# Kernel tuning notes

Hardware: AMD Instinct MI355X
Metric: run time of the kernel (lower is better)

The kernel has to match this reference:

```python
import jax, jax.numpy as jnp
import numpy as np

B, S, T = 128, 512, 256


def setup_inputs() -> dict:
    key = jax.random.key(0)
    k1, k2, k3, k4 = jax.random.split(key, 4)
    emissions = jax.random.normal(k1, (B, S, T), dtype=jnp.float32)
    mask = jnp.ones((B, S), dtype=bool)
    transitions = jax.random.normal(k2, (T, T), dtype=jnp.float32)
    start_transitions = jax.random.normal(k3, (T,), dtype=jnp.float32)
    end_transitions = jax.random.normal(k4, (T,), dtype=jnp.float32)
    return {
        "emissions": emissions,
        "mask": mask,
        "transitions": transitions,
        "start_transitions": start_transitions,
        "end_transitions": end_transitions,
    }


def reference(emissions, mask, transitions, start_transitions, end_transitions):
    """Batched Viterbi decode. Returns (paths [B,S] int32, best_scores [B] f32).

    Faithful to CRFLayer._viterbi_decode: score_0 = start + em_0; at each step
    next[i,j] = score[i] + trans[i,j] + em_t[j], take max/argmax over i; add
    end_transitions at the end; backtrack via backpointers. Masked (padded)
    steps carry score through unchanged with identity backpointers, so padded
    tail positions replicate the last valid tag (mask is all-ones here, so
    output equals the original's full-length paths).
    """
    Bn, Sn, Tn = emissions.shape
    ident = jnp.arange(Tn, dtype=jnp.int32)
    score0 = start_transitions[None, :] + emissions[:, 0]  # [B,T]

    em_ts = jnp.swapaxes(emissions, 0, 1)[1:]  # [S-1,B,T]
    m_ts = jnp.swapaxes(mask, 0, 1)[1:]        # [S-1,B]

    def step(score, inp):
        em_t, m_t = inp
        # nxt[b,i,j] = score[b,i] + trans[i,j] + em_t[b,j]
        nxt = score[:, :, None] + transitions[None, :, :] + em_t[:, None, :]
        best = jnp.max(nxt, axis=1)                    # [B,T]
        idx = jnp.argmax(nxt, axis=1).astype(jnp.int32)  # [B,T] best prev tag
        m = m_t[:, None]
        new_score = jnp.where(m, best, score)
        bp = jnp.where(m, idx, ident[None, :])
        return new_score, bp

    final_score, history = jax.lax.scan(step, score0, (em_ts, m_ts))  # history [S-1,B,T]
    final_score = final_score + end_transitions[None, :]
    best_scores = jnp.max(final_score, axis=1)                         # [B]
    last_tag = jnp.argmax(final_score, axis=1).astype(jnp.int32)       # [B]

    def back(tag, hist_t):
        prev = jnp.take_along_axis(hist_t, tag[:, None], axis=1)[:, 0]
        return prev, tag  # carry prev tag, emit current tag

    first_tag, tags_rest = jax.lax.scan(back, last_tag, history, reverse=True)
    # tags_rest[t] = tag at position t+1; first_tag = tag at position 0
    paths = jnp.concatenate([first_tag[:, None], jnp.swapaxes(tags_rest, 0, 1)], axis=1)
    return paths, best_scores
```

## Files before the change

### kernel.cpp

```cpp
#include <hip/hip_runtime.h>

#define Bn 128
#define Sn 512
#define Tn 256

typedef float v4f __attribute__((ext_vector_type(4)));

__device__ __forceinline__ void barrier_lgkm() {
  asm volatile("s_waitcnt lgkmcnt(0)\n\ts_barrier" ::: "memory");
}

template <int CTRL>
__device__ __forceinline__ float dpp_fmax(float v) {
  int x = __builtin_amdgcn_mov_dpp(__float_as_int(v), CTRL, 0xF, 0xF, true);
  return fmaxf(v, __int_as_float(x));
}
__device__ __forceinline__ float row_fmax16(float v) {
  v = dpp_fmax<0x128>(v);
  v = dpp_fmax<0x124>(v);
  v = dpp_fmax<0x122>(v);
  v = dpp_fmax<0x121>(v);
  return v;
}
__device__ __forceinline__ float wave_fmax64(float v) {
  v = row_fmax16(v);
  int x = __builtin_amdgcn_ds_swizzle(__float_as_int(v), 0x401F);
  v = fmaxf(v, __int_as_float(x));
  v = fmaxf(v, __shfl_xor(v, 32));
  return v;
}
__device__ __forceinline__ float readlane_f(float v, int l) {
  return __int_as_float(__builtin_amdgcn_readlane(__float_as_int(v), l));
}
__device__ __forceinline__ float sel4(v4f v, int c) {
  return (c == 0) ? v.x : (c == 1) ? v.y : (c == 2) ? v.z : v.w;
}

__global__ __launch_bounds__(256) void transpose_kernel(
    const float* __restrict__ tr, float* __restrict__ trT) {
  int idx = blockIdx.x * 256 + threadIdx.x;
  int i = idx >> 8;
  int j = idx & 255;
  trT[j * Tn + i] = tr[i * Tn + j];
}

__global__ __launch_bounds__(1024, 4) void viterbi_fwd(
    const float* __restrict__ em,
    const float* __restrict__ trans,
    const float* __restrict__ start,
    float* __restrict__ scores)
{
  const int b    = blockIdx.x;
  const int tid  = threadIdx.x;
  const int lane = tid & 63;
  const int w    = tid >> 6;
  const int ip   = lane >> 2;
  const int jq   = lane & 3;
  const int jbase = w * 16 + jq * 4;
  const int i0    = ip * 16;
  const int b2 = (lane >> 2) & 1;
  const int b3 = (lane >> 3) & 1;
  const int myc = jbase + b2 * 2 + b3;
  const bool writer = (lane & 48) == 0;

  __shared__ float sbuf[2][Tn];

  float4 tr[16];
#pragma unroll
  for (int k = 0; k < 16; ++k)
    tr[k] = *reinterpret_cast<const float4*>(trans + (i0 + k) * Tn + jbase);

  const float* emb = em + (size_t)b * Sn * Tn;
  float* scb = scores + (size_t)b * Sn * Tn;

  if (tid < 64) {
    int j4 = tid * 4;
    float4 st = *reinterpret_cast<const float4*>(start + j4);
    float4 e0 = *reinterpret_cast<const float4*>(emb + j4);
    float4 s0 = make_float4(st.x + e0.x, st.y + e0.y, st.z + e0.z, st.w + e0.w);
    *reinterpret_cast<float4*>(&sbuf[0][j4]) = s0;
    *reinterpret_cast<float4*>(scb + j4) = s0;
  }

  const float* em_pre = emb + 2 * Tn + myc;
  float*       sc_w   = scb + Tn + myc;
  float e_cur = 0.0f;
  if (writer) e_cur = emb[Tn + myc];
  barrier_lgkm();

  int cur = 0;
  for (int t = 1; t < Sn; ++t) {
    const float* sp = &sbuf[cur][i0];
    float4 a0 = *reinterpret_cast<const float4*>(sp);
    float4 a1 = *reinterpret_cast<const float4*>(sp + 4);
    float4 a2 = *reinterpret_cast<const float4*>(sp + 8);
    float4 a3 = *reinterpret_cast<const float4*>(sp + 12);

    float e_nxt = 0.0f;
    if (writer) {
      const float* p = (t + 1 < Sn) ? em_pre : em_pre - Tn;
      e_nxt = *p;
    }

    float se[16] = {a0.x,a0.y,a0.z,a0.w, a1.x,a1.y,a1.z,a1.w,
                    a2.x,a2.y,a2.z,a2.w, a3.x,a3.y,a3.z,a3.w};

    float m0 = fmaxf(fmaxf(se[0]+tr[0].x, se[1]+tr[1].x), se[2]+tr[2].x);
    float m1 = fmaxf(fmaxf(se[0]+tr[0].y, se[1]+tr[1].y), se[2]+tr[2].y);
    float m2 = fmaxf(fmaxf(se[0]+tr[0].z, se[1]+tr[1].z), se[2]+tr[2].z);
    float m3 = fmaxf(fmaxf(se[0]+tr[0].w, se[1]+tr[1].w), se[2]+tr[2].w);
#pragma unroll
    for (int k = 3; k < 15; k += 2) {
      m0 = fmaxf(fmaxf(m0, se[k]+tr[k].x), se[k+1]+tr[k+1].x);
      m1 = fmaxf(fmaxf(m1, se[k]+tr[k].y), se[k+1]+tr[k+1].y);
      m2 = fmaxf(fmaxf(m2, se[k]+tr[k].z), se[k+1]+tr[k+1].z);
      m3 = fmaxf(fmaxf(m3, se[k]+tr[k].w), se[k+1]+tr[k+1].w);
    }
    m0 = fmaxf(m0, se[15]+tr[15].x);
    m1 = fmaxf(m1, se[15]+tr[15].y);
    m2 = fmaxf(m2, se[15]+tr[15].z);
    m3 = fmaxf(m3, se[15]+tr[15].w);

    float sA = b2 ? m0 : m2;
    float rA = __shfl_xor(sA, 4);
    float sB = b2 ? m1 : m3;
    float rB = __shfl_xor(sB, 4);
    float p0 = fmaxf(b2 ? m2 : m0, rA);
    float p1 = fmaxf(b2 ? m3 : m1, rB);
    float sC = b3 ? p0 : p1;
    float rC = __shfl_xor(sC, 8);
    float q  = fmaxf(b3 ? p1 : p0, rC);
    q = fmaxf(q, __shfl_xor(q, 16));
    q = fmaxf(q, __shfl_xor(q, 32));

    if (writer) {
      float ns = q + e_cur;
      sbuf[cur ^ 1][myc] = ns;
      *sc_w = ns;
    }
    e_cur = e_nxt;
    em_pre += Tn;
    sc_w   += Tn;
    cur ^= 1;
    barrier_lgkm();
  }
}

__global__ __launch_bounds__(128, 1) void viterbi_bwd(
    const float* __restrict__ em,
    const float* __restrict__ trT,
    const float* __restrict__ endt,
    const float* __restrict__ scores,
    float* __restrict__ out)
{
  const int b = blockIdx.x;
  const int tid = threadIdx.x;
  const int lane = tid & 63;
  const float* scb = scores + (size_t)b * Sn * Tn;
  const float* emb = em + (size_t)b * Sn * Tn;
  const int base = lane * 4;
  const int BIG = 1 << 30;

  __shared__ unsigned char pbuf[Sn];
  __shared__ int done;

  if (tid == 0) done = 0;
  __syncthreads();

  if (tid < 64) {
    float4 s = *reinterpret_cast<const float4*>(scb + (size_t)(Sn - 1) * Tn + base);
    float4 e = *reinterpret_cast<const float4*>(endt + base);
    float d0 = s.x + e.x;
    float d1 = s.y + e.y;
    float d2 = s.z + e.z;
    float d3 = s.w + e.w;
    float bv = fmaxf(fmaxf(fmaxf(d0, d1), d2), d3);
    bv = wave_fmax64(bv);
    int li = BIG;
    if (d3 == bv) li = base + 3;
    if (d2 == bv) li = base + 2;
    if (d1 == bv) li = base + 1;
    if (d0 == bv) li = base;
    unsigned long long mk = __ballot(li != BIG);
    int tag = __shfl(li, (int)__ffsll((long long)mk) - 1);
    if (lane == 0) {
      out[Bn * Sn + b] = bv;
      pbuf[Sn - 1] = (unsigned char)tag;
    }
    tag = __builtin_amdgcn_readfirstlane(tag);

    #define LD_V4(ptr) __builtin_nontemporal_load(reinterpret_cast<const v4f*>(ptr))

    v4f S0, S1, S2, S3, E0, E1, E2, E3;
    S3 = LD_V4(scb + (size_t)(Sn - 1) * Tn + base);
    E3 = LD_V4(emb + (size_t)(Sn - 1) * Tn + base);
    S2 = LD_V4(scb + (size_t)(Sn - 2) * Tn + base);
    E2 = LD_V4(emb + (size_t)(Sn - 2) * Tn + base);
    S1 = LD_V4(scb + (size_t)(Sn - 3) * Tn + base);
    E1 = LD_V4(emb + (size_t)(Sn - 3) * Tn + base);

    #define BWD_STEP(kk_, SP_, SC_, SN_, EP_, EN_) {                           \
      const int k_ = (kk_);                                                    \
                      \
      float4 tv = *reinterpret_cast<const float4*>(trT + (size_t)tag * Tn + base); \
      __builtin_amdgcn_sched_barrier(0);                                       \
              \
      int kp_ = (k_ >= 2) ? k_ - 2 : 0;                                        \
      SN_ = LD_V4(scb + (size_t)kp_ * Tn + base);                              \
      EN_ = LD_V4(emb + (size_t)kp_ * Tn + base);                              \
      __builtin_amdgcn_sched_barrier(0);                                       \
                    \
      int comp_ = tag & 3;                                                     \
      float dmax_ = readlane_f(sel4(SP_, comp_), tag >> 2);                    \
      float ev_   = readlane_f(sel4(EP_, comp_), tag >> 2);                    \
         \
      float c0_ = (SC_.x + tv.x) + ev_;                                        \
      float c1_ = (SC_.y + tv.y) + ev_;                                        \
      float c2_ = (SC_.z + tv.z) + ev_;                                        \
      float c3_ = (SC_.w + tv.w) + ev_;                                        \
      unsigned long long m0_ = __ballot(c0_ == dmax_);                         \
      unsigned long long m1_ = __ballot(c1_ == dmax_);                         \
      unsigned long long m2_ = __ballot(c2_ == dmax_);                         \
      unsigned long long m3_ = __ballot(c3_ == dmax_);                         \
      int f0_ = (int)__ffsll((long long)m0_);                                  \
      int f1_ = (int)__ffsll((long long)m1_);                                  \
      int f2_ = (int)__ffsll((long long)m2_);                                  \
      int f3_ = (int)__ffsll((long long)m3_);                                  \
      int i0_ = f0_ ? ((f0_ - 1) * 4 + 0) : BIG;                               \
      int i1_ = f1_ ? ((f1_ - 1) * 4 + 1) : BIG;                               \
      int i2_ = f2_ ? ((f2_ - 1) * 4 + 2) : BIG;                               \
      int i3_ = f3_ ? ((f3_ - 1) * 4 + 3) : BIG;                               \
      int ta_ = (i0_ < i1_) ? i0_ : i1_;                                       \
      int tb_ = (i2_ < i3_) ? i2_ : i3_;                                       \
      tag = (ta_ < tb_) ? ta_ : tb_;                                           \
      tag = __builtin_amdgcn_readfirstlane(tag);                               \
      if (lane == 0) pbuf[k_] = (unsigned char)tag;                            \
    }

    for (int kk = Sn - 2; kk >= 3; kk -= 4) {
      BWD_STEP(kk,     S3, S2, S0, E3, E0);
      BWD_STEP(kk - 1, S2, S1, S3, E2, E3);
      BWD_STEP(kk - 2, S1, S0, S2, E1, E2);
      BWD_STEP(kk - 3, S0, S3, S1, E0, E1);
    }
    BWD_STEP(2, S3, S2, S0, E3, E0);
    BWD_STEP(1, S2, S1, S3, E2, E3);
    BWD_STEP(0, S1, S0, S2, E1, E2);

    #undef BWD_STEP
    #undef LD_V4

    __threadfence_block();
    *(volatile int*)&done = 1;
  } else {
    volatile int* dp = &done;
    const int wbase = lane * 4;
    int off = wbase;
    while (true) {
      #pragma unroll
      for (int c = 0; c < 2; ++c) {
        float4 w0 = *reinterpret_cast<const float4*>(trT + off);
        float4 w1 = *reinterpret_cast<const float4*>(trT + off + 256);
        float4 w2 = *reinterpret_cast<const float4*>(trT + off + 512);
        float4 w3 = *reinterpret_cast<const float4*>(trT + off + 768);
        asm volatile("" :: "v"(w0.x), "v"(w1.x), "v"(w2.x), "v"(w3.x));
        off += 1024;
        if (off >= Tn * Tn) off = wbase;
      }
      if (*dp != 0) break;
    }
  }

  __syncthreads();
  if (tid < 64)
    for (int s2 = lane; s2 < Sn; s2 += 64)
      out[(size_t)b * Sn + s2] = (float)pbuf[s2];
}

extern "C" void kernel_launch(void* const* d_in, const int* in_sizes, int n_in,
                              void* d_out, int out_size, void* d_ws, size_t ws_size,
                              hipStream_t stream) {
  const float* em    = (const float*)d_in[0];
  const float* trans = (const float*)d_in[2];
  const float* start = (const float*)d_in[3];
  const float* endt  = (const float*)d_in[4];
  float* out = (float*)d_out;

  float* scores = (float*)d_ws;
  float* trT = (float*)((char*)d_ws + (size_t)Bn * Sn * Tn * 4);

  transpose_kernel<<<Tn * Tn / 256, 256, 0, stream>>>(trans, trT);
  viterbi_fwd<<<Bn, 1024, 0, stream>>>(em, trans, start, scores);
  viterbi_bwd<<<Bn, 128, 0, stream>>>(em, trT, endt, scores, out);
}
```

Measured before the change: 618.0 us.

## Stage part of transitions in LDS and deepen backtrack prefetch to eight steps

Copies the first 152 rows of the transposed transition matrix into shared memory with async global-to-LDS loads, so backtrack steps whose tag falls in that range read from LDS instead of global memory. The score and emission prefetch ring grows from 4 to 8 registers, prefetching six steps ahead. The helper wave that keeps the transitions warm in cache now cycles only over the rows not held in LDS. The tag-dependent branch adds divergence-free but data-dependent latency variation, and the large LDS allocation and extra registers may limit occupancy.

```diff
diff --git a/kernel.cpp b/kernel.cpp
--- a/kernel.cpp
+++ b/kernel.cpp
@@ -3,8 +3,16 @@
 #define Bn 128
 #define Sn 512
 #define Tn 256
+#define NROWS 152
 
 typedef float v4f __attribute__((ext_vector_type(4)));
+
+typedef __attribute__((address_space(3))) unsigned int lds_u32_t;
+typedef __attribute__((address_space(1))) unsigned int glb_u32_t;
+
+__device__ __forceinline__ void gl_lds16(const float* g, float* l) {
+  __builtin_amdgcn_global_load_lds((const glb_u32_t*)g, (lds_u32_t*)l, 16, 0, 0);
+}
 
 __device__ __forceinline__ void barrier_lgkm() {
   asm volatile("s_waitcnt lgkmcnt(0)\n\ts_barrier" ::: "memory");
@@ -161,10 +169,18 @@
   const int base = lane * 4;
   const int BIG = 1 << 30;
 
+  __shared__ float ldsT[NROWS * Tn];
   __shared__ unsigned char pbuf[Sn];
   __shared__ int done;
 
   if (tid == 0) done = 0;
+
+  {
+    const int r0 = (tid < 64) ? 0 : NROWS / 2;
+    const int r1 = (tid < 64) ? NROWS / 2 : NROWS;
+    for (int r = r0; r < r1; ++r)
+      gl_lds16(trT + (size_t)r * Tn + base, &ldsT[r * Tn]);
+  }
   __syncthreads();
 
   if (tid < 64) {
@@ -191,21 +207,35 @@
 
     #define LD_V4(ptr) __builtin_nontemporal_load(reinterpret_cast<const v4f*>(ptr))
 
-    v4f S0, S1, S2, S3, E0, E1, E2, E3;
-    S3 = LD_V4(scb + (size_t)(Sn - 1) * Tn + base);
-    E3 = LD_V4(emb + (size_t)(Sn - 1) * Tn + base);
-    S2 = LD_V4(scb + (size_t)(Sn - 2) * Tn + base);
-    E2 = LD_V4(emb + (size_t)(Sn - 2) * Tn + base);
-    S1 = LD_V4(scb + (size_t)(Sn - 3) * Tn + base);
-    E1 = LD_V4(emb + (size_t)(Sn - 3) * Tn + base);
+    v4f S0, S1, S2, S3, S4, S5, S6, S7;
+    v4f E0, E1, E2, E3, E4, E5, E6, E7;
+    S7 = LD_V4(scb + (size_t)(Sn - 1) * Tn + base);
+    E7 = LD_V4(emb + (size_t)(Sn - 1) * Tn + base);
+    S6 = LD_V4(scb + (size_t)(Sn - 2) * Tn + base);
+    E6 = LD_V4(emb + (size_t)(Sn - 2) * Tn + base);
+    S5 = LD_V4(scb + (size_t)(Sn - 3) * Tn + base);
+    E5 = LD_V4(emb + (size_t)(Sn - 3) * Tn + base);
+    S4 = LD_V4(scb + (size_t)(Sn - 4) * Tn + base);
+    E4 = LD_V4(emb + (size_t)(Sn - 4) * Tn + base);
+    S3 = LD_V4(scb + (size_t)(Sn - 5) * Tn + base);
+    E3 = LD_V4(emb + (size_t)(Sn - 5) * Tn + base);
+    S2 = LD_V4(scb + (size_t)(Sn - 6) * Tn + base);
+    E2 = LD_V4(emb + (size_t)(Sn - 6) * Tn + base);
+    S1 = LD_V4(scb + (size_t)(Sn - 7) * Tn + base);
+    E1 = LD_V4(emb + (size_t)(Sn - 7) * Tn + base);
 
     #define BWD_STEP(kk_, SP_, SC_, SN_, EP_, EN_) {                           \
       const int k_ = (kk_);                                                    \
-                      \
-      float4 tv = *reinterpret_cast<const float4*>(trT + (size_t)tag * Tn + base); \
+           \
+      float4 tv;                                                               \
+      if (tag < NROWS) {                                                       \
+        tv = *reinterpret_cast<const float4*>(&ldsT[tag * Tn + base]);         \
+      } else {                                                                 \
+        tv = *reinterpret_cast<const float4*>(trT + (size_t)tag * Tn + base);  \
+      }                                                                        \
       __builtin_amdgcn_sched_barrier(0);                                       \
               \
-      int kp_ = (k_ >= 2) ? k_ - 2 : 0;                                        \
+      int kp_ = (k_ >= 6) ? k_ - 6 : 0;                                        \
       SN_ = LD_V4(scb + (size_t)kp_ * Tn + base);                              \
       EN_ = LD_V4(emb + (size_t)kp_ * Tn + base);                              \
       __builtin_amdgcn_sched_barrier(0);                                       \
@@ -237,13 +267,21 @@
       if (lane == 0) pbuf[k_] = (unsigned char)tag;                            \
     }
 
-    for (int kk = Sn - 2; kk >= 3; kk -= 4) {
-      BWD_STEP(kk,     S3, S2, S0, E3, E0);
-      BWD_STEP(kk - 1, S2, S1, S3, E2, E3);
-      BWD_STEP(kk - 2, S1, S0, S2, E1, E2);
-      BWD_STEP(kk - 3, S0, S3, S1, E0, E1);
-    }
-    BWD_STEP(2, S3, S2, S0, E3, E0);
+    for (int kk = Sn - 2; kk >= 14; kk -= 8) {
+      BWD_STEP(kk,     S7, S6, S0, E7, E0);
+      BWD_STEP(kk - 1, S6, S5, S7, E6, E7);
+      BWD_STEP(kk - 2, S5, S4, S6, E5, E6);
+      BWD_STEP(kk - 3, S4, S3, S5, E4, E5);
+      BWD_STEP(kk - 4, S3, S2, S4, E3, E4);
+      BWD_STEP(kk - 5, S2, S1, S3, E2, E3);
+      BWD_STEP(kk - 6, S1, S0, S2, E1, E2);
+      BWD_STEP(kk - 7, S0, S7, S1, E0, E1);
+    }
+    BWD_STEP(6, S7, S6, S0, E7, E0);
+    BWD_STEP(5, S6, S5, S7, E6, E7);
+    BWD_STEP(4, S5, S4, S6, E5, E6);
+    BWD_STEP(3, S4, S3, S5, E4, E5);
+    BWD_STEP(2, S3, S2, S4, E3, E4);
     BWD_STEP(1, S2, S1, S3, E2, E3);
     BWD_STEP(0, S1, S0, S2, E1, E2);
 
@@ -254,20 +292,15 @@
     *(volatile int*)&done = 1;
   } else {
     volatile int* dp = &done;
-    const int wbase = lane * 4;
-    int off = wbase;
-    while (true) {
-      #pragma unroll
-      for (int c = 0; c < 2; ++c) {
+    while (*dp == 0) {
+      for (int off = NROWS * Tn + base; off < Tn * Tn; off += 1024) {
         float4 w0 = *reinterpret_cast<const float4*>(trT + off);
         float4 w1 = *reinterpret_cast<const float4*>(trT + off + 256);
         float4 w2 = *reinterpret_cast<const float4*>(trT + off + 512);
         float4 w3 = *reinterpret_cast<const float4*>(trT + off + 768);
         asm volatile("" :: "v"(w0.x), "v"(w1.x), "v"(w2.x), "v"(w3.x));
-        off += 1024;
-        if (off >= Tn * Tn) off = wbase;
+        if (*dp != 0) break;
       }
-      if (*dp != 0) break;
     }
   }
 
```

Measured after the change: 697.6 us. 12.9% more time.
